# Kernel tuning notes

Measured on AMD Instinct MI355X. Metric: run time of the kernel, lower is better.

The kernel has to match this reference:

```python
import jax, jax.numpy as jnp
import numpy as np

B, T, N, F_IN = 32, 64, 128, 16
H, SOUT = 64, 16
D = N * SOUT            # transformer d_model = 2048
NHEADS, DH = 16, 128
DFF, LAYERS = 2048, 2
NCLASSES, OUT = 8, 10
THR = 0.004             # edge threshold on sigmoid(V)/N


def setup_inputs():
    key = jax.random.key(0)
    ks = iter(jax.random.split(key, 40))
    r = lambda *s: jax.random.normal(next(ks), s, jnp.float32) * 0.02
    return {
        'X': jax.random.normal(next(ks), (B, T, N * F_IN), jnp.float32),
        'V_Adap': jax.random.normal(next(ks), (NCLASSES, N, N), jnp.float32),
        'Wl': r(F_IN, H), 'bl': jnp.zeros((H,)),
        'Wr': r(F_IN, H), 'br': jnp.zeros((H,)),
        'att': jax.random.normal(next(ks), (H,), jnp.float32) * 0.1,
        'gat_bias': jnp.zeros((H,)),
        'Wfc': r(H, SOUT), 'bfc': jnp.zeros((SOUT,)),
        'Wq': r(LAYERS, D, D), 'bq': jnp.zeros((LAYERS, D)),
        'Wk': r(LAYERS, D, D), 'bk': jnp.zeros((LAYERS, D)),
        'Wv': r(LAYERS, D, D), 'bv': jnp.zeros((LAYERS, D)),
        'Wo': r(LAYERS, D, D), 'bo': jnp.zeros((LAYERS, D)),
        'ln1_g': jnp.ones((LAYERS, D)), 'ln1_b': jnp.zeros((LAYERS, D)),
        'W1': r(LAYERS, D, DFF), 'b1': jnp.zeros((LAYERS, DFF)),
        'W2': r(LAYERS, DFF, D), 'b2': jnp.zeros((LAYERS, D)),
        'ln2_g': jnp.ones((LAYERS, D)), 'ln2_b': jnp.zeros((LAYERS, D)),
        'Wout': r(D, OUT), 'bout': jnp.zeros((OUT,)),
        'class_idx': 2,
    }


def _ln(x, g, b):
    mu = jnp.mean(x, -1, keepdims=True)
    var = jnp.var(x, -1, keepdims=True)
    return (x - mu) / jnp.sqrt(var + 1e-5) * g + b


def reference(X, V_Adap, Wl, bl, Wr, br, att, gat_bias, Wfc, bfc,
              Wq, bq, Wk, bk, Wv, bv, Wo, bo, ln1_g, ln1_b,
              W1, b1, W2, b2, ln2_g, ln2_b, Wout, bout, class_idx):
    # dynamic adjacency: sigmoid + scale + threshold (data-dependent sparsity as a mask)
    A = jax.nn.sigmoid(V_Adap[class_idx]) / N
    mask = (A > THR) | jnp.eye(N, dtype=bool)   # GATv2Conv default add_self_loops

    def gat_step(x_t):                           # x_t: (B, N, F_IN)
        xl = x_t @ Wl + bl                       # source transform (B, N, H)
        xr = x_t @ Wr + br                       # target transform (B, N, H)
        s = jax.nn.leaky_relu(xl[:, :, None, :] + xr[:, None, :, :], 0.2)  # (B, src, dst, H)
        e = jnp.where(mask[None], jnp.einsum('bijh,h->bij', s, att), -1e9)
        alpha = jax.nn.softmax(e, axis=1)        # softmax over sources per target node
        out = jnp.einsum('bij,bih->bjh', alpha, xl) + gat_bias
        return out @ Wfc + bfc                   # (B, N, SOUT)

    Xr = X.reshape(B, T, N, F_IN).transpose(1, 0, 2, 3)   # (T, B, N, F)
    spatial = jax.lax.map(gat_step, Xr)                   # (T, B, N, SOUT)
    h = spatial.transpose(1, 0, 2, 3).reshape(B, T, D)

    # post-norm TransformerEncoder (torch defaults: relu, d_ff=2048, no dropout at eval)
    for l in range(LAYERS):
        q = (h @ Wq[l] + bq[l]).reshape(B, T, NHEADS, DH).transpose(0, 2, 1, 3)
        k = (h @ Wk[l] + bk[l]).reshape(B, T, NHEADS, DH).transpose(0, 2, 1, 3)
        v = (h @ Wv[l] + bv[l]).reshape(B, T, NHEADS, DH).transpose(0, 2, 1, 3)
        aw = jax.nn.softmax(jnp.einsum('bhqd,bhkd->bhqk', q, k) / np.float32(np.sqrt(DH)), axis=-1)
        ao = jnp.einsum('bhqk,bhkd->bhqd', aw, v).transpose(0, 2, 1, 3).reshape(B, T, D)
        h = _ln(h + ao @ Wo[l] + bo[l], ln1_g[l], ln1_b[l])
        ff = jax.nn.relu(h @ W1[l] + b1[l]) @ W2[l] + b2[l]
        h = _ln(h + ff, ln2_g[l], ln2_b[l])

    return h[:, -1, :] @ Wout + bout             # (B, OUT)
```

## Files before the change

### kernel.cpp

```cpp
#include <hip/hip_runtime.h>
#include <cstdint>
#include <cstddef>


typedef unsigned short u16;
typedef __bf16 bf16x8 __attribute__((ext_vector_type(8)));
typedef float f32x4 __attribute__((ext_vector_type(4)));
typedef float f32x2 __attribute__((ext_vector_type(2)));
typedef unsigned int u32x4 __attribute__((ext_vector_type(4)));
typedef float f32x4v __attribute__((ext_vector_type(4)));
typedef unsigned short u16x4 __attribute__((ext_vector_type(4)));

__device__ __forceinline__ u16 f2b(float f) {
  union { float f; unsigned u; } x; x.f = f;
  unsigned r = x.u + 0x7fffu + ((x.u >> 16) & 1u);
  return (u16)(r >> 16);
}
__device__ __forceinline__ float b2f(u16 s) {
  union { unsigned u; float f; } x; x.u = ((unsigned)s) << 16;
  return x.f;
}
__device__ __forceinline__ float b2f_lo(unsigned q) {
  union { unsigned u; float f; } x; x.u = q << 16;
  return x.f;
}
__device__ __forceinline__ float b2f_hi(unsigned q) {
  union { unsigned u; float f; } x; x.u = q & 0xffff0000u;
  return x.f;
}

__device__ __forceinline__ void gload_lds16(const void* g, void* l) {
  __builtin_amdgcn_global_load_lds(
      (const __attribute__((address_space(1))) unsigned int*)g,
      (__attribute__((address_space(3))) unsigned int*)l, 16, 0, 0);
}

__global__ __launch_bounds__(1024) void gat_kernel(
    const float* __restrict__ X, const float* __restrict__ V_Adap,
    const int* __restrict__ class_idx,
    const float* __restrict__ Wl, const float* __restrict__ bl,
    const float* __restrict__ Wr, const float* __restrict__ br,
    const float* __restrict__ att, const float* __restrict__ gat_bias,
    const float* __restrict__ Wfc, const float* __restrict__ bfc,
    float* __restrict__ h_f32, u16* __restrict__ h_b16)
{
  const int bt = blockIdx.x;
  const int tid = threadIdx.x;

  __shared__ __align__(16) float xlT[64 * 132];
  __shared__ __align__(16) float xrT[64 * 132];
  __shared__ __align__(16) u16   xlTb[64 * 136];
  __shared__ __align__(16) u16   esbT[128 * 136];
  __shared__ __align__(16) u16   aggb[128 * 72];
  __shared__ __align__(16) float WlT[64 * 20];
  __shared__ __align__(16) float WrT[64 * 20];
  __shared__ __align__(16) float WfcT[16 * 66];
  __shared__ float atts[64], bls[64], brs[64], gbias[64], bfcs[16];
  __shared__ float cls[128], crs[128], inv_s[128];
  __shared__ float red[8 * 128];

  float* scratchX = (float*)aggb;

  {
    const int h = tid >> 4, f = tid & 15;
    WlT[h * 20 + f] = Wl[f * 64 + h];
    WrT[h * 20 + f] = Wr[f * 64 + h];
    WfcT[f * 66 + h] = Wfc[h * 16 + f];
  }
  if (tid < 64) { atts[tid] = att[tid]; bls[tid] = bl[tid]; brs[tid] = br[tid]; gbias[tid] = gat_bias[tid]; }
  if (tid < 16) bfcs[tid] = bfc[tid];
  if (tid < 512)
    ((f32x4*)scratchX)[tid] = ((const f32x4*)(X + (size_t)bt * 2048))[tid];
  const int cidx = *class_idx;
  __syncthreads();

  {
    const int h = tid & 63, ng = tid >> 6;
    f32x4 wl4[4], wr4[4];
    #pragma unroll
    for (int f4 = 0; f4 < 4; f4++) {
      wl4[f4] = *(const f32x4*)&WlT[h * 20 + f4 * 4];
      wr4[f4] = *(const f32x4*)&WrT[h * 20 + f4 * 4];
    }
    const float blh = bls[h], brh = brs[h];
    float al8[8], ar8[8];
    #pragma unroll
    for (int t = 0; t < 8; t++) {
      const int n = ng * 8 + t;
      float al = blh, ar = brh;
      #pragma unroll
      for (int f4 = 0; f4 < 4; f4++) {
        const f32x4 xv = *(const f32x4*)&scratchX[n * 16 + f4 * 4];
        #pragma unroll
        for (int f = 0; f < 4; f++) {
          al = fmaf(xv[f], wl4[f4][f], al);
          ar = fmaf(xv[f], wr4[f4][f], ar);
        }
      }
      al8[t] = al; ar8[t] = ar;
    }
    *(f32x4*)&xlT[h * 132 + ng * 8]     = *(f32x4*)&al8[0];
    *(f32x4*)&xlT[h * 132 + ng * 8 + 4] = *(f32x4*)&al8[4];
    *(f32x4*)&xrT[h * 132 + ng * 8]     = *(f32x4*)&ar8[0];
    *(f32x4*)&xrT[h * 132 + ng * 8 + 4] = *(f32x4*)&ar8[4];
    u16 pb[8];
    #pragma unroll
    for (int t = 0; t < 8; t++) pb[t] = f2b(al8[t]);
    *(u16x4*)&xlTb[h * 136 + ng * 8]     = *(u16x4*)&pb[0];
    *(u16x4*)&xlTb[h * 136 + ng * 8 + 4] = *(u16x4*)&pb[4];
  }
  __syncthreads();

  {
    const int n = tid & 127, g = tid >> 7;
    const float* srcT = (g < 4) ? xlT : xrT;
    const int h0 = (g & 3) * 16;
    float s = 0.f;
    #pragma unroll
    for (int hh = 0; hh < 16; hh++)
      s = fmaf(atts[h0 + hh], srcT[(h0 + hh) * 132 + n], s);
    red[g * 128 + n] = s;
  }
  __syncthreads();
  if (tid < 256) {
    const int n = tid & 127;
    const int base = (tid < 128) ? 0 : 4;
    const float s = ((red[base * 128 + n] + red[(base + 1) * 128 + n])
                   + red[(base + 2) * 128 + n]) + red[(base + 3) * 128 + n];
    if (tid < 128) cls[n] = s; else crs[n] = s;
  }
  __syncthreads();

  {
    const int i0 = (tid >> 6) * 8;
    const int j0 = (tid & 63) * 2;
    float acc[8][2] = {};
    #pragma unroll 8
    for (int h = 0; h < 64; h++) {
      const float ah = att[h];
      const f32x4 xa0 = *(const f32x4*)&xlT[h * 132 + i0];
      const f32x4 xa1 = *(const f32x4*)&xlT[h * 132 + i0 + 4];
      const f32x2 xb  = *(const f32x2*)&xrT[h * 132 + j0];
      #pragma unroll
      for (int a = 0; a < 4; a++) {
        acc[a][0]     = fmaf(ah, __builtin_fabsf(xa0[a] + xb[0]), acc[a][0]);
        acc[a][1]     = fmaf(ah, __builtin_fabsf(xa0[a] + xb[1]), acc[a][1]);
        acc[4 + a][0] = fmaf(ah, __builtin_fabsf(xa1[a] + xb[0]), acc[4 + a][0]);
        acc[4 + a][1] = fmaf(ah, __builtin_fabsf(xa1[a] + xb[1]), acc[4 + a][1]);
      }
    }
    const float* Vc = V_Adap + (size_t)cidx * 16384;
    float vm[8][2];
    #pragma unroll
    for (int a = 0; a < 8; a++) {
      const f32x2 vc = *(const f32x2*)&Vc[(size_t)(i0 + a) * 128 + j0];
      vm[a][0] = vc[0]; vm[a][1] = vc[1];
    }
    const f32x4 cl0 = *(const f32x4*)&cls[i0];
    const f32x4 cl1 = *(const f32x4*)&cls[i0 + 4];
    float cli[8] = {cl0[0], cl0[1], cl0[2], cl0[3], cl1[0], cl1[1], cl1[2], cl1[3]};
    #pragma unroll
    for (int b = 0; b < 2; b++) {
      const int j = j0 + b;
      const float ej = 0.6f * crs[j];
      u16 pk[8];
      #pragma unroll
      for (int a = 0; a < 8; a++) {
        const int i = i0 + a;
        const float e = ej + 0.6f * cli[a] + 0.4f * acc[a][b];
        const bool m = (vm[a][b] > 0.04800922f) || (i == j);
        pk[a] = f2b(m ? e : -1e9f);
      }
      *(u16x4*)&esbT[j * 136 + i0]     = *(u16x4*)&pk[0];
      *(u16x4*)&esbT[j * 136 + i0 + 4] = *(u16x4*)&pk[4];
    }
  }
  __syncthreads();

  {
    const int j = tid >> 3, c = tid & 7;
    u16* rp = &esbT[j * 136 + c * 16];
    float ps = 0.f;
    #pragma unroll
    for (int half = 0; half < 2; half++) {
      u32x4 q = *(u32x4*)(rp + half * 8);
      #pragma unroll
      for (int w2 = 0; w2 < 4; w2++) {
        const float p0 = __expf(b2f_lo(q[w2]));
        const float p1 = __expf(b2f_hi(q[w2]));
        ps += p0 + p1;
        q[w2] = (unsigned)f2b(p0) | ((unsigned)f2b(p1) << 16);
      }
      *(u32x4*)(rp + half * 8) = q;
    }
    red[c * 128 + j] = ps;
  }
  __syncthreads();
  if (tid < 128) {
    float s = 0.f;
    #pragma unroll
    for (int c = 0; c < 8; c++) s += red[c * 128 + tid];
    inv_s[tid] = 1.f / s;
  }
  __syncthreads();

  {
    const int w = tid >> 6, lane = tid & 63;
    const int lq = lane >> 4, lr = lane & 15;
    const int jt = w >> 1, ht0 = (w & 1) * 2;
    f32x4 acc2[2] = {};
    #pragma unroll
    for (int ks = 0; ks < 4; ks++) {
      const bf16x8 af = __builtin_bit_cast(bf16x8,
          *(const u32x4*)&esbT[(jt * 16 + lr) * 136 + ks * 32 + lq * 8]);
      #pragma unroll
      for (int t = 0; t < 2; t++) {
        const bf16x8 bfb = __builtin_bit_cast(bf16x8,
            *(const u32x4*)&xlTb[((ht0 + t) * 16 + lr) * 136 + ks * 32 + lq * 8]);
        acc2[t] = __builtin_amdgcn_mfma_f32_16x16x32_bf16(af, bfb, acc2[t], 0, 0, 0);
      }
    }
    #pragma unroll
    for (int t = 0; t < 2; t++) {
      const int h = (ht0 + t) * 16 + lr;
      const float gb = gbias[h];
      #pragma unroll
      for (int r = 0; r < 4; r++) {
        const int j = jt * 16 + lq * 4 + r;
        aggb[j * 72 + h] = f2b(acc2[t][r] * inv_s[j] + gb);
      }
    }
  }
  __syncthreads();

  {
    const int j = tid >> 3, s0 = (tid & 7) * 2;
    float o0 = bfcs[s0], o1 = bfcs[s0 + 1];
    #pragma unroll
    for (int h8 = 0; h8 < 8; h8++) {
      u32x4 q = *(const u32x4*)&aggb[j * 72 + h8 * 8];
      #pragma unroll
      for (int w2 = 0; w2 < 4; w2++) {
        const int h = h8 * 8 + w2 * 2;
        const float a0 = b2f_lo(q[w2]);
        const float a1 = b2f_hi(q[w2]);
        o0 = fmaf(a0, WfcT[s0 * 66 + h], o0);
        o1 = fmaf(a0, WfcT[(s0 + 1) * 66 + h], o1);
        o0 = fmaf(a1, WfcT[s0 * 66 + h + 1], o0);
        o1 = fmaf(a1, WfcT[(s0 + 1) * 66 + h + 1], o1);
      }
    }
    const size_t off = (size_t)bt * 2048 + j * 16 + s0;
    h_f32[off] = o0; h_f32[off + 1] = o1;
    h_b16[off] = f2b(o0); h_b16[off + 1] = f2b(o1);
  }
}

struct TransArgs {
  const float* s0; const float* s1; const float* s2;
  u16* d0; u16* d1; u16* d2;
};

__global__ __launch_bounds__(256) void transpose_cast(TransArgs p)
{
  const float* src = (blockIdx.z == 0) ? p.s0 : (blockIdx.z == 1) ? p.s1 : p.s2;
  u16* dst = (blockIdx.z == 0) ? p.d0 : (blockIdx.z == 1) ? p.d1 : p.d2;
  __shared__ u16 tile[64][66];
  const int k0 = blockIdx.y * 64, n0 = blockIdx.x * 64;
  const int tid = threadIdx.x;
  const int c = tid & 63, rb = tid >> 6;
  #pragma unroll
  for (int r = 0; r < 16; r++) {
    const int k = rb + r * 4;
    tile[k][c] = f2b(src[(size_t)(k0 + k) * 2048 + n0 + c]);
  }
  __syncthreads();
  #pragma unroll
  for (int r = 0; r < 16; r++) {
    const int n = rb + r * 4;
    dst[(size_t)(n0 + n) * 2048 + k0 + c] = tile[c][n];
  }
}

struct GemmArgs {
  const u16* A;
  const u16* Bt0; const u16* Bt1; const u16* Bt2;
  const float* b0; const float* b1; const float* b2;
  void* C0; void* C1; void* C2;
  int N; int K;
};

template <int MODE>
__global__ __launch_bounds__(256) void gemm_bt(GemmArgs g)
{
  const int z = blockIdx.z;
  const u16* Bt = (z == 0) ? g.Bt0 : (z == 1) ? g.Bt1 : g.Bt2;
  const float* bias = (z == 0) ? g.b0 : (z == 1) ? g.b1 : g.b2;
  void* C = (z == 0) ? g.C0 : (z == 1) ? g.C1 : g.C2;
  const int N = g.N, K = g.K;
  const int m0 = blockIdx.y * 128, n0 = blockIdx.x * 128;

  __shared__ __align__(16) u16 As[3][128 * 32];
  __shared__ __align__(16) u16 Bs[3][128 * 32];

  const int tid = threadIdx.x;
  const int lane = tid & 63, w = tid >> 6;
  const int srow = w * 16 + (lane >> 2);
  const int scol = ((lane & 3) ^ ((lane >> 2) & 3)) * 8;
  const u16* gA = g.A + (size_t)(m0 + srow) * K + scol;
  const u16* gB = Bt + (size_t)(n0 + srow) * K + scol;
  const int lbase = (w * 16) * 32;

  const int wm = (w >> 1) * 64, wn = (w & 1) * 64;
  const int lq = lane >> 4, lr = lane & 15;
  const int csw = (lr & 3) << 3;

  f32x4 acc[4][4] = {};
  const int NT = K >> 5;

  auto stage = [&](int buf, int kt) {
    const int kk = kt << 5;
    #pragma unroll
    for (int c = 0; c < 2; c++) {
      gload_lds16(gA + (size_t)(c * 64) * K + kk, &As[buf][lbase + c * 64 * 32]);
      gload_lds16(gB + (size_t)(c * 64) * K + kk, &Bs[buf][lbase + c * 64 * 32]);
    }
  };
  auto compute = [&](int buf) {
    bf16x8 af[4], bfr[4];
    #pragma unroll
    for (int i = 0; i < 4; i++) {
      af[i] = __builtin_bit_cast(bf16x8,
          *(const u32x4*)&As[buf][(wm + i * 16 + lr) * 32 + ((lq * 8) ^ csw)]);
      bfr[i] = __builtin_bit_cast(bf16x8,
          *(const u32x4*)&Bs[buf][(wn + i * 16 + lr) * 32 + ((lq * 8) ^ csw)]);
    }
    #pragma unroll
    for (int mi = 0; mi < 4; mi++)
      #pragma unroll
      for (int ni = 0; ni < 4; ni++)
        acc[mi][ni] = __builtin_amdgcn_mfma_f32_16x16x32_bf16(af[mi], bfr[ni], acc[mi][ni], 0, 0, 0);
  };

  stage(0, 0);
  stage(1, 1);
  int cA = 0;
  for (int kt = 0; kt < NT; ++kt) {
    if (kt + 2 < NT) {
      int b2 = cA + 2; if (b2 >= 3) b2 -= 3;
      stage(b2, kt + 2);
      asm volatile("s_waitcnt vmcnt(8)" ::: "memory");
    } else if (kt + 1 < NT) {
      asm volatile("s_waitcnt vmcnt(4)" ::: "memory");
    } else {
      asm volatile("s_waitcnt vmcnt(0)" ::: "memory");
    }
    __builtin_amdgcn_s_barrier();
    asm volatile("" ::: "memory");
    __builtin_amdgcn_s_setprio(1);
    compute(cA);
    __builtin_amdgcn_s_setprio(0);
    asm volatile("" ::: "memory");
    __builtin_amdgcn_s_barrier();
    asm volatile("" ::: "memory");
    if (++cA == 3) cA = 0;
  }

  #pragma unroll
  for (int ni = 0; ni < 4; ni++) {
    const int col = n0 + wn + ni * 16 + lr;
    const float bv = bias[col];
    #pragma unroll
    for (int mi = 0; mi < 4; mi++) {
      #pragma unroll
      for (int r = 0; r < 4; r++) {
        const int row = m0 + wm + mi * 16 + lq * 4 + r;
        float v = acc[mi][ni][r] + bv;
        if (MODE == 0) {
          ((float*)C)[(size_t)row * N + col] = v;
        } else {
          if (MODE == 2) v = fmaxf(v, 0.f);
          ((u16*)C)[(size_t)row * N + col] = f2b(v);
        }
      }
    }
  }
}

template <int MODE>
__global__ __launch_bounds__(256) void gemm_bt64(GemmArgs g)
{
  const u16* Bt = g.Bt0;
  const float* bias = g.b0;
  void* C = g.C0;
  const int N = g.N, K = g.K;
  const int m0 = blockIdx.y * 128, n0 = blockIdx.x * 64;

  __shared__ __align__(16) u16 As[3][128 * 64];
  __shared__ __align__(16) u16 Bs[3][64 * 64];

  const int tid = threadIdx.x;
  const int lane = tid & 63, w = tid >> 6;
  const int srow = w * 8 + (lane >> 3);
  const int scol = ((lane & 7) ^ (lane >> 3)) * 8;
  const u16* gA = g.A + (size_t)(m0 + srow) * K + scol;
  const u16* gB = Bt + (size_t)(n0 + srow) * K + scol;
  const int lbase = (w * 8) * 64;

  const int wm = w * 32;
  const int lq = lane >> 4, lr = lane & 15;
  const int csw = (lr & 7) << 3;

  f32x4 acc[2][4] = {};
  const int NT = K >> 6;

  auto stage = [&](int buf, int kt) {
    const int kk = kt << 6;
    #pragma unroll
    for (int c = 0; c < 4; c++)
      gload_lds16(gA + (size_t)(c * 32) * K + kk, &As[buf][lbase + c * 32 * 64]);
    #pragma unroll
    for (int c = 0; c < 2; c++)
      gload_lds16(gB + (size_t)(c * 32) * K + kk, &Bs[buf][lbase + c * 32 * 64]);
  };
  auto compute = [&](int buf) {
    #pragma unroll
    for (int ks = 0; ks < 2; ks++) {
      bf16x8 af[2], bfr[4];
      #pragma unroll
      for (int i = 0; i < 2; i++)
        af[i] = __builtin_bit_cast(bf16x8,
            *(const u32x4*)&As[buf][(wm + i * 16 + lr) * 64 + ((ks * 32 + lq * 8) ^ csw)]);
      #pragma unroll
      for (int i = 0; i < 4; i++)
        bfr[i] = __builtin_bit_cast(bf16x8,
            *(const u32x4*)&Bs[buf][(i * 16 + lr) * 64 + ((ks * 32 + lq * 8) ^ csw)]);
      #pragma unroll
      for (int mi = 0; mi < 2; mi++)
        #pragma unroll
        for (int ni = 0; ni < 4; ni++)
          acc[mi][ni] = __builtin_amdgcn_mfma_f32_16x16x32_bf16(af[mi], bfr[ni], acc[mi][ni], 0, 0, 0);
    }
  };

  stage(0, 0);
  stage(1, 1);
  int cA = 0;
  for (int kt = 0; kt < NT; ++kt) {
    if (kt + 2 < NT) {
      int b2 = cA + 2; if (b2 >= 3) b2 -= 3;
      stage(b2, kt + 2);
      asm volatile("s_waitcnt vmcnt(12)" ::: "memory");
    } else if (kt + 1 < NT) {
      asm volatile("s_waitcnt vmcnt(6)" ::: "memory");
    } else {
      asm volatile("s_waitcnt vmcnt(0)" ::: "memory");
    }
    __builtin_amdgcn_s_barrier();
    asm volatile("" ::: "memory");
    __builtin_amdgcn_s_setprio(1);
    compute(cA);
    __builtin_amdgcn_s_setprio(0);
    asm volatile("" ::: "memory");
    __builtin_amdgcn_s_barrier();
    asm volatile("" ::: "memory");
    if (++cA == 3) cA = 0;
  }

  #pragma unroll
  for (int ni = 0; ni < 4; ni++) {
    const int col = n0 + ni * 16 + lr;
    const float bv = bias[col];
    #pragma unroll
    for (int mi = 0; mi < 2; mi++) {
      #pragma unroll
      for (int r = 0; r < 4; r++) {
        const int row = m0 + wm + mi * 16 + lq * 4 + r;
        float v = acc[mi][ni][r] + bv;
        if (MODE == 0) {
          ((float*)C)[(size_t)row * N + col] = v;
        } else {
          if (MODE == 2) v = fmaxf(v, 0.f);
          ((u16*)C)[(size_t)row * N + col] = f2b(v);
        }
      }
    }
  }
}

__global__ __launch_bounds__(256) void attn_kernel(
    const u16* __restrict__ Qb, const u16* __restrict__ Kb,
    const u16* __restrict__ Vb, u16* __restrict__ AOb)
{
  const int head = blockIdx.x, b = blockIdx.y;
  const int tid = threadIdx.x;
  __shared__ __align__(16) float qs[64 * 132];
  __shared__ __align__(16) float ks[64 * 132];
  __shared__ __align__(16) float vs[64 * 128];
  __shared__ __align__(16) float ss[64 * 65];
  const size_t base = ((size_t)b * 64) * 2048 + (size_t)head * 128;

  for (int idx = tid; idx < 1024; idx += 256) {
    const int t_ = idx >> 4, d8 = (idx & 15) * 8;
    const size_t gp = base + (size_t)t_ * 2048 + d8;
    const u32x4 q = *(const u32x4*)(Qb + gp);
    const u32x4 k = *(const u32x4*)(Kb + gp);
    const u32x4 v = *(const u32x4*)(Vb + gp);
    f32x4 q0 = {b2f_lo(q[0]), b2f_hi(q[0]), b2f_lo(q[1]), b2f_hi(q[1])};
    f32x4 q1 = {b2f_lo(q[2]), b2f_hi(q[2]), b2f_lo(q[3]), b2f_hi(q[3])};
    f32x4 k0 = {b2f_lo(k[0]), b2f_hi(k[0]), b2f_lo(k[1]), b2f_hi(k[1])};
    f32x4 k1 = {b2f_lo(k[2]), b2f_hi(k[2]), b2f_lo(k[3]), b2f_hi(k[3])};
    f32x4 v0 = {b2f_lo(v[0]), b2f_hi(v[0]), b2f_lo(v[1]), b2f_hi(v[1])};
    f32x4 v1 = {b2f_lo(v[2]), b2f_hi(v[2]), b2f_lo(v[3]), b2f_hi(v[3])};
    *(f32x4*)&qs[t_ * 132 + d8] = q0; *(f32x4*)&qs[t_ * 132 + d8 + 4] = q1;
    *(f32x4*)&ks[t_ * 132 + d8] = k0; *(f32x4*)&ks[t_ * 132 + d8 + 4] = k1;
    *(f32x4*)&vs[t_ * 128 + d8] = v0; *(f32x4*)&vs[t_ * 128 + d8 + 4] = v1;
  }
  __syncthreads();

  {
    const int i0 = (tid >> 4) * 4, j0 = tid & 15;
    float acc[4][4] = {};
    #pragma unroll 2
    for (int d0 = 0; d0 < 128; d0 += 4) {
      f32x4 qv[4], kv[4];
      #pragma unroll
      for (int a = 0; a < 4; a++) qv[a] = *(const f32x4*)&qs[(i0 + a) * 132 + d0];
      #pragma unroll
      for (int c = 0; c < 4; c++) kv[c] = *(const f32x4*)&ks[(j0 + c * 16) * 132 + d0];
      #pragma unroll
      for (int a = 0; a < 4; a++)
        #pragma unroll
        for (int c = 0; c < 4; c++)
          #pragma unroll
          for (int e = 0; e < 4; e++)
            acc[a][c] = fmaf(qv[a][e], kv[c][e], acc[a][c]);
    }
    const float sc = 0.08838834764831845f;
    #pragma unroll
    for (int a = 0; a < 4; a++)
      #pragma unroll
      for (int c = 0; c < 4; c++)
        ss[(i0 + a) * 65 + j0 + c * 16] = acc[a][c] * sc;
  }
  __syncthreads();

  {
    const int row = tid >> 2;
    float* rp = &ss[row * 65 + (tid & 3) * 16];
    float mx = -3e38f;
    #pragma unroll
    for (int j = 0; j < 16; j++) mx = fmaxf(mx, rp[j]);
    mx = fmaxf(mx, __shfl_xor(mx, 1, 64));
    mx = fmaxf(mx, __shfl_xor(mx, 2, 64));
    float s = 0.f;
    #pragma unroll
    for (int j = 0; j < 16; j++) { const float p = __expf(rp[j] - mx); rp[j] = p; s += p; }
    s += __shfl_xor(s, 1, 64);
    s += __shfl_xor(s, 2, 64);
    const float inv = 1.f / s;
    #pragma unroll
    for (int j = 0; j < 16; j++) rp[j] *= inv;
  }
  __syncthreads();

  {
    const int i0 = (tid >> 4) * 4, d0 = (tid & 15) * 8;
    float o[4][8] = {};
    for (int j = 0; j < 64; j++) {
      float pv[4];
      #pragma unroll
      for (int a = 0; a < 4; a++) pv[a] = ss[(i0 + a) * 65 + j];
      f32x4v v0 = *(const f32x4v*)&vs[j * 128 + d0];
      f32x4v v1 = *(const f32x4v*)&vs[j * 128 + d0 + 4];
      float vv[8] = {v0[0], v0[1], v0[2], v0[3], v1[0], v1[1], v1[2], v1[3]};
      #pragma unroll
      for (int a = 0; a < 4; a++)
        #pragma unroll
        for (int c = 0; c < 8; c++)
          o[a][c] = fmaf(pv[a], vv[c], o[a][c]);
    }
    #pragma unroll
    for (int a = 0; a < 4; a++)
      #pragma unroll
      for (int c = 0; c < 8; c++)
        AOb[base + (size_t)(i0 + a) * 2048 + d0 + c] = f2b(o[a][c]);
  }
}

__global__ __launch_bounds__(256) void ln_kernel(
    const float* __restrict__ hin, const float* __restrict__ delta,
    const float* __restrict__ gamma, const float* __restrict__ beta,
    float* __restrict__ hout, u16* __restrict__ bout_)
{
  const int token = blockIdx.x, tid = threadIdx.x;
  const size_t off = (size_t)token * 2048;
  __shared__ float red[8];
  f32x4 v[2];
  float s = 0.f;
  #pragma unroll
  for (int r = 0; r < 2; r++) {
    const int i = r * 1024 + tid * 4;
    const f32x4 a = *(const f32x4*)(hin + off + i);
    const f32x4 b = *(const f32x4*)(delta + off + i);
    v[r] = a + b;
    s += v[r][0] + v[r][1] + v[r][2] + v[r][3];
  }
  #pragma unroll
  for (int o = 32; o > 0; o >>= 1) s += __shfl_down(s, o, 64);
  if ((tid & 63) == 0) red[tid >> 6] = s;
  __syncthreads();
  const float mean = (red[0] + red[1] + red[2] + red[3]) * (1.f / 2048.f);
  float s2 = 0.f;
  #pragma unroll
  for (int r = 0; r < 2; r++)
    #pragma unroll
    for (int e = 0; e < 4; e++) { const float d = v[r][e] - mean; s2 = fmaf(d, d, s2); }
  #pragma unroll
  for (int o = 32; o > 0; o >>= 1) s2 += __shfl_down(s2, o, 64);
  if ((tid & 63) == 0) red[4 + (tid >> 6)] = s2;
  __syncthreads();
  const float var = (red[4] + red[5] + red[6] + red[7]) * (1.f / 2048.f);
  const float rstd = rsqrtf(var + 1e-5f);
  #pragma unroll
  for (int r = 0; r < 2; r++) {
    const int i = r * 1024 + tid * 4;
    const f32x4 gm = *(const f32x4*)(gamma + i);
    const f32x4 bt = *(const f32x4*)(beta + i);
    f32x4 y;
    u16x4 pb;
    #pragma unroll
    for (int e = 0; e < 4; e++) {
      y[e] = (v[r][e] - mean) * rstd * gm[e] + bt[e];
      pb[e] = f2b(y[e]);
    }
    *(f32x4*)(hout + off + i) = y;
    *(u16x4*)(bout_ + off + i) = pb;
  }
}

__global__ __launch_bounds__(256) void final_kernel(
    const float* __restrict__ h, const float* __restrict__ Wout,
    const float* __restrict__ bout, float* __restrict__ out)
{
  const int b = blockIdx.x, tid = threadIdx.x;
  __shared__ float row[2048];
  __shared__ float part[256];
  const float* hr = h + ((size_t)b * 64 + 63) * 2048;
  for (int i = tid; i < 2048; i += 256) row[i] = hr[i];
  __syncthreads();
  const int o = tid & 15, ch = tid >> 4;
  float s = 0.f;
  if (o < 10) {
    const int i0 = ch * 128;
    for (int i = i0; i < i0 + 128; i++) s = fmaf(row[i], Wout[(size_t)i * 10 + o], s);
  }
  part[tid] = s;
  __syncthreads();
  if (tid < 10) {
    float t = bout[tid];
    for (int c2 = 0; c2 < 16; c2++) t += part[c2 * 16 + tid];
    out[(size_t)b * 10 + tid] = t;
  }
}

extern "C" void kernel_launch(void* const* d_in, const int* in_sizes, int n_in,
                              void* d_out, int out_size, void* d_ws, size_t ws_size,
                              hipStream_t stream)
{
  const float* X        = (const float*)d_in[0];
  const float* V_Adap   = (const float*)d_in[1];
  const float* Wl       = (const float*)d_in[2];
  const float* bl       = (const float*)d_in[3];
  const float* Wr       = (const float*)d_in[4];
  const float* br       = (const float*)d_in[5];
  const float* att      = (const float*)d_in[6];
  const float* gat_bias = (const float*)d_in[7];
  const float* Wfc      = (const float*)d_in[8];
  const float* bfc      = (const float*)d_in[9];
  const float* Wq       = (const float*)d_in[10];
  const float* bq       = (const float*)d_in[11];
  const float* Wk       = (const float*)d_in[12];
  const float* bk       = (const float*)d_in[13];
  const float* Wv       = (const float*)d_in[14];
  const float* bv       = (const float*)d_in[15];
  const float* Wo       = (const float*)d_in[16];
  const float* bo       = (const float*)d_in[17];
  const float* ln1_g    = (const float*)d_in[18];
  const float* ln1_b    = (const float*)d_in[19];
  const float* W1       = (const float*)d_in[20];
  const float* b1       = (const float*)d_in[21];
  const float* W2       = (const float*)d_in[22];
  const float* b2       = (const float*)d_in[23];
  const float* ln2_g    = (const float*)d_in[24];
  const float* ln2_b    = (const float*)d_in[25];
  const float* WoutP    = (const float*)d_in[26];
  const float* boutP    = (const float*)d_in[27];
  const int*   class_idx = (const int*)d_in[28];

  char* ws = (char*)d_ws;
  const size_t MB = (size_t)1 << 20;
  float* h_f32 = (float*)(ws);
  u16*   h_b16 = (u16*)(ws + 16 * MB);
  u16*   Qb    = (u16*)(ws + 24 * MB);
  u16*   Kb    = (u16*)(ws + 32 * MB);
  u16*   Vb    = (u16*)(ws + 40 * MB);
  u16*   AOb   = (u16*)(ws + 48 * MB);
  float* tmp   = (float*)(ws + 56 * MB);
  u16*   ff1b  = (u16*)(ws + 72 * MB);
  u16*   Wt0   = (u16*)(ws + 80 * MB);
  u16*   Wt1   = (u16*)(ws + 88 * MB);
  u16*   Wt2   = (u16*)(ws + 96 * MB);

  gat_kernel<<<2048, 1024, 0, stream>>>(X, V_Adap, class_idx, Wl, bl, Wr, br,
                                        att, gat_bias, Wfc, bfc, h_f32, h_b16);

  const size_t DD = 2048ull * 2048ull;
  for (int l = 0; l < 2; l++) {
    const size_t wofs = (size_t)l * DD;
    const size_t bofs = (size_t)l * 2048;

    transpose_cast<<<dim3(32, 32, 3), 256, 0, stream>>>(
        TransArgs{Wq + wofs, Wk + wofs, Wv + wofs, Wt0, Wt1, Wt2});
    gemm_bt<1><<<dim3(16, 16, 3), 256, 0, stream>>>(
        GemmArgs{h_b16, Wt0, Wt1, Wt2, bq + bofs, bk + bofs, bv + bofs,
                 Qb, Kb, Vb, 2048, 2048});

    attn_kernel<<<dim3(16, 32), 256, 0, stream>>>(Qb, Kb, Vb, AOb);

    transpose_cast<<<dim3(32, 32, 3), 256, 0, stream>>>(
        TransArgs{Wo + wofs, W1 + wofs, W2 + wofs, Wt0, Wt1, Wt2});

    gemm_bt64<0><<<dim3(32, 16), 256, 0, stream>>>(
        GemmArgs{AOb, Wt0, nullptr, nullptr, bo + bofs, nullptr, nullptr,
                 tmp, nullptr, nullptr, 2048, 2048});
    ln_kernel<<<2048, 256, 0, stream>>>(h_f32, tmp, ln1_g + bofs, ln1_b + bofs,
                                        h_f32, h_b16);

    gemm_bt64<2><<<dim3(32, 16), 256, 0, stream>>>(
        GemmArgs{h_b16, Wt1, nullptr, nullptr, b1 + bofs, nullptr, nullptr,
                 ff1b, nullptr, nullptr, 2048, 2048});

    gemm_bt64<0><<<dim3(32, 16), 256, 0, stream>>>(
        GemmArgs{ff1b, Wt2, nullptr, nullptr, b2 + bofs, nullptr, nullptr,
                 tmp, nullptr, nullptr, 2048, 2048});
    ln_kernel<<<2048, 256, 0, stream>>>(h_f32, tmp, ln2_g + bofs, ln2_b + bofs,
                                        h_f32, h_b16);
  }

  final_kernel<<<32, 256, 0, stream>>>(h_f32, WoutP, boutP, (float*)d_out);
}
```

Before: 874.4 us.

## Split-K output GEMMs, swizzle GEMM grids, MFMA attention scores, fuse GAT softmax exp

Several independent changes land together. The Wo and W2 projections now use a new split-K GEMM (gemm_bt64sk) that writes two fp32 partial sums, and the LayerNorm kernel adds both partials into the residual. This doubles the number of blocks for those GEMMs. Both existing GEMMs get a blockIdx swizzle that groups tiles for better L2 reuse. Attention QK^T now keeps Q and K in bf16 shared memory and computes scores with MFMA instead of scalar fp32 FMAs. In the GAT kernel the exp and masking move into the edge-score pass, which drops one shared-memory pass and one barrier. The exp now runs on the unshifted scores with no max subtraction, and the attention scores lose some precision from bf16.

```diff
diff --git a/kernel.cpp b/kernel.cpp
--- a/kernel.cpp
+++ b/kernel.cpp
@@ -60,6 +60,7 @@
   __shared__ float red[8 * 128];
 
   float* scratchX = (float*)aggb;
+  float* red2 = (float*)aggb;
 
   {
     const int h = tid >> 4, f = tid & 15;
@@ -132,7 +133,8 @@
   __syncthreads();
 
   {
-    const int i0 = (tid >> 6) * 8;
+    const int w = tid >> 6;
+    const int i0 = w * 8;
     const int j0 = (tid & 63) * 2;
     float acc[8][2] = {};
     #pragma unroll 8
@@ -159,47 +161,33 @@
     const f32x4 cl0 = *(const f32x4*)&cls[i0];
     const f32x4 cl1 = *(const f32x4*)&cls[i0 + 4];
     float cli[8] = {cl0[0], cl0[1], cl0[2], cl0[3], cl1[0], cl1[1], cl1[2], cl1[3]};
+    float psum[2];
     #pragma unroll
     for (int b = 0; b < 2; b++) {
       const int j = j0 + b;
       const float ej = 0.6f * crs[j];
       u16 pk[8];
+      float ps = 0.f;
       #pragma unroll
       for (int a = 0; a < 8; a++) {
         const int i = i0 + a;
         const float e = ej + 0.6f * cli[a] + 0.4f * acc[a][b];
         const bool m = (vm[a][b] > 0.04800922f) || (i == j);
-        pk[a] = f2b(m ? e : -1e9f);
-      }
+        const float p = m ? __expf(e) : 0.f;
+        ps += p;
+        pk[a] = f2b(p);
+      }
+      psum[b] = ps;
       *(u16x4*)&esbT[j * 136 + i0]     = *(u16x4*)&pk[0];
       *(u16x4*)&esbT[j * 136 + i0 + 4] = *(u16x4*)&pk[4];
     }
-  }
-  __syncthreads();
-
-  {
-    const int j = tid >> 3, c = tid & 7;
-    u16* rp = &esbT[j * 136 + c * 16];
-    float ps = 0.f;
-    #pragma unroll
-    for (int half = 0; half < 2; half++) {
-      u32x4 q = *(u32x4*)(rp + half * 8);
-      #pragma unroll
-      for (int w2 = 0; w2 < 4; w2++) {
-        const float p0 = __expf(b2f_lo(q[w2]));
-        const float p1 = __expf(b2f_hi(q[w2]));
-        ps += p0 + p1;
-        q[w2] = (unsigned)f2b(p0) | ((unsigned)f2b(p1) << 16);
-      }
-      *(u32x4*)(rp + half * 8) = q;
-    }
-    red[c * 128 + j] = ps;
+    *(f32x2*)&red2[w * 128 + j0] = *(f32x2*)&psum[0];
   }
   __syncthreads();
   if (tid < 128) {
     float s = 0.f;
     #pragma unroll
-    for (int c = 0; c < 8; c++) s += red[c * 128 + tid];
+    for (int c = 0; c < 16; c++) s += red2[c * 128 + tid];
     inv_s[tid] = 1.f / s;
   }
   __syncthreads();
@@ -298,7 +286,11 @@
   const float* bias = (z == 0) ? g.b0 : (z == 1) ? g.b1 : g.b2;
   void* C = (z == 0) ? g.C0 : (z == 1) ? g.C1 : g.C2;
   const int N = g.N, K = g.K;
-  const int m0 = blockIdx.y * 128, n0 = blockIdx.x * 128;
+  const int lin = blockIdx.y * 16 + blockIdx.x;
+  const int xc = lin & 7, xt = lin >> 3;
+  const int wx = (xc & 3) * 4 + (xt & 3);
+  const int wy = (xc >> 2) * 8 + (xt >> 2);
+  const int m0 = wy * 128, n0 = wx * 128;
 
   __shared__ __align__(16) u16 As[3][128 * 32];
   __shared__ __align__(16) u16 Bs[3][128 * 32];
@@ -394,7 +386,11 @@
   const float* bias = g.b0;
   void* C = g.C0;
   const int N = g.N, K = g.K;
-  const int m0 = blockIdx.y * 128, n0 = blockIdx.x * 64;
+  const int lin = blockIdx.y * 32 + blockIdx.x;
+  const int xc = lin & 7, xt = lin >> 3;
+  const int wx = (xc & 3) * 8 + (xt & 7);
+  const int wy = (xc >> 2) * 8 + (xt >> 3);
+  const int m0 = wy * 128, n0 = wx * 64;
 
   __shared__ __align__(16) u16 As[3][128 * 64];
   __shared__ __align__(16) u16 Bs[3][64 * 64];
@@ -488,14 +484,109 @@
   }
 }
 
+__global__ __launch_bounds__(256) void gemm_bt64sk(
+    const u16* __restrict__ A, const u16* __restrict__ Bt,
+    const float* __restrict__ bias, float* __restrict__ C0,
+    float* __restrict__ C1, int N, int K)
+{
+  const int z = blockIdx.z;
+  float* C = z ? C1 : C0;
+  const int khalf = K >> 1;
+  const int lin = blockIdx.y * 32 + blockIdx.x;
+  const int xc = lin & 7, xt = lin >> 3;
+  const int wx = (xc & 3) * 8 + (xt & 7);
+  const int wy = (xc >> 2) * 8 + (xt >> 3);
+  const int m0 = wy * 128, n0 = wx * 64;
+
+  __shared__ __align__(16) u16 As[3][128 * 32];
+  __shared__ __align__(16) u16 Bs[3][64 * 32];
+
+  const int tid = threadIdx.x;
+  const int lane = tid & 63, w = tid >> 6;
+  const int srow = w * 16 + (lane >> 2);
+  const int scol = ((lane & 3) ^ ((lane >> 2) & 3)) * 8;
+  const u16* gA = A + (size_t)(m0 + srow) * K + (size_t)z * khalf + scol;
+  const u16* gB = Bt + (size_t)(n0 + srow) * K + (size_t)z * khalf + scol;
+  const int lbaseA = (w * 16) * 32;
+  const int lbaseB = (w * 16) * 32;
+
+  const int wm = w * 32;
+  const int lq = lane >> 4, lr = lane & 15;
+  const int csw = (lr & 3) << 3;
+
+  f32x4 acc[2][4] = {};
+  const int NT = khalf >> 5;
+
+  auto stage = [&](int buf, int kt) {
+    const int kk = kt << 5;
+    gload_lds16(gA + kk, &As[buf][lbaseA]);
+    gload_lds16(gA + (size_t)64 * K + kk, &As[buf][lbaseA + 64 * 32]);
+    gload_lds16(gB + kk, &Bs[buf][lbaseB]);
+  };
+  auto compute = [&](int buf) {
+    bf16x8 af[2], bfr[4];
+    #pragma unroll
+    for (int i = 0; i < 2; i++)
+      af[i] = __builtin_bit_cast(bf16x8,
+          *(const u32x4*)&As[buf][(wm + i * 16 + lr) * 32 + ((lq * 8) ^ csw)]);
+    #pragma unroll
+    for (int i = 0; i < 4; i++)
+      bfr[i] = __builtin_bit_cast(bf16x8,
+          *(const u32x4*)&Bs[buf][(i * 16 + lr) * 32 + ((lq * 8) ^ csw)]);
+    #pragma unroll
+    for (int mi = 0; mi < 2; mi++)
+      #pragma unroll
+      for (int ni = 0; ni < 4; ni++)
+        acc[mi][ni] = __builtin_amdgcn_mfma_f32_16x16x32_bf16(af[mi], bfr[ni], acc[mi][ni], 0, 0, 0);
+  };
+
+  stage(0, 0);
+  stage(1, 1);
+  int cA = 0;
+  for (int kt = 0; kt < NT; ++kt) {
+    if (kt + 2 < NT) {
+      int b2 = cA + 2; if (b2 >= 3) b2 -= 3;
+      stage(b2, kt + 2);
+      asm volatile("s_waitcnt vmcnt(6)" ::: "memory");
+    } else if (kt + 1 < NT) {
+      asm volatile("s_waitcnt vmcnt(3)" ::: "memory");
+    } else {
+      asm volatile("s_waitcnt vmcnt(0)" ::: "memory");
+    }
+    __builtin_amdgcn_s_barrier();
+    asm volatile("" ::: "memory");
+    __builtin_amdgcn_s_setprio(1);
+    compute(cA);
+    __builtin_amdgcn_s_setprio(0);
+    asm volatile("" ::: "memory");
+    __builtin_amdgcn_s_barrier();
+    asm volatile("" ::: "memory");
+    if (++cA == 3) cA = 0;
+  }
+
+  #pragma unroll
+  for (int ni = 0; ni < 4; ni++) {
+    const int col = n0 + ni * 16 + lr;
+    const float bv = z ? 0.f : bias[col];
+    #pragma unroll
+    for (int mi = 0; mi < 2; mi++) {
+      #pragma unroll
+      for (int r = 0; r < 4; r++) {
+        const int row = m0 + wm + mi * 16 + lq * 4 + r;
+        C[(size_t)row * N + col] = acc[mi][ni][r] + bv;
+      }
+    }
+  }
+}
+
 __global__ __launch_bounds__(256) void attn_kernel(
     const u16* __restrict__ Qb, const u16* __restrict__ Kb,
     const u16* __restrict__ Vb, u16* __restrict__ AOb)
 {
   const int head = blockIdx.x, b = blockIdx.y;
   const int tid = threadIdx.x;
-  __shared__ __align__(16) float qs[64 * 132];
-  __shared__ __align__(16) float ks[64 * 132];
+  __shared__ __align__(16) u16   qs16[64 * 136];
+  __shared__ __align__(16) u16   ks16[64 * 136];
   __shared__ __align__(16) float vs[64 * 128];
   __shared__ __align__(16) float ss[64 * 65];
   const size_t base = ((size_t)b * 64) * 2048 + (size_t)head * 128;
@@ -506,42 +597,35 @@
     const u32x4 q = *(const u32x4*)(Qb + gp);
     const u32x4 k = *(const u32x4*)(Kb + gp);
     const u32x4 v = *(const u32x4*)(Vb + gp);
-    f32x4 q0 = {b2f_lo(q[0]), b2f_hi(q[0]), b2f_lo(q[1]), b2f_hi(q[1])};
-    f32x4 q1 = {b2f_lo(q[2]), b2f_hi(q[2]), b2f_lo(q[3]), b2f_hi(q[3])};
-    f32x4 k0 = {b2f_lo(k[0]), b2f_hi(k[0]), b2f_lo(k[1]), b2f_hi(k[1])};
-    f32x4 k1 = {b2f_lo(k[2]), b2f_hi(k[2]), b2f_lo(k[3]), b2f_hi(k[3])};
+    *(u32x4*)&qs16[t_ * 136 + d8] = q;
+    *(u32x4*)&ks16[t_ * 136 + d8] = k;
     f32x4 v0 = {b2f_lo(v[0]), b2f_hi(v[0]), b2f_lo(v[1]), b2f_hi(v[1])};
     f32x4 v1 = {b2f_lo(v[2]), b2f_hi(v[2]), b2f_lo(v[3]), b2f_hi(v[3])};
-    *(f32x4*)&qs[t_ * 132 + d8] = q0; *(f32x4*)&qs[t_ * 132 + d8 + 4] = q1;
-    *(f32x4*)&ks[t_ * 132 + d8] = k0; *(f32x4*)&ks[t_ * 132 + d8 + 4] = k1;
     *(f32x4*)&vs[t_ * 128 + d8] = v0; *(f32x4*)&vs[t_ * 128 + d8 + 4] = v1;
   }
   __syncthreads();
 
   {
-    const int i0 = (tid >> 4) * 4, j0 = tid & 15;
-    float acc[4][4] = {};
-    #pragma unroll 2
-    for (int d0 = 0; d0 < 128; d0 += 4) {
-      f32x4 qv[4], kv[4];
-      #pragma unroll
-      for (int a = 0; a < 4; a++) qv[a] = *(const f32x4*)&qs[(i0 + a) * 132 + d0];
-      #pragma unroll
-      for (int c = 0; c < 4; c++) kv[c] = *(const f32x4*)&ks[(j0 + c * 16) * 132 + d0];
-      #pragma unroll
-      for (int a = 0; a < 4; a++)
-        #pragma unroll
-        for (int c = 0; c < 4; c++)
-          #pragma unroll
-          for (int e = 0; e < 4; e++)
-            acc[a][c] = fmaf(qv[a][e], kv[c][e], acc[a][c]);
+    const int w = tid >> 6, lane = tid & 63;
+    const int lq = lane >> 4, lr = lane & 15;
+    f32x4 acc4[4] = {};
+    #pragma unroll
+    for (int ks = 0; ks < 4; ks++) {
+      const bf16x8 kf = __builtin_bit_cast(bf16x8,
+          *(const u32x4*)&ks16[(w * 16 + lr) * 136 + ks * 32 + lq * 8]);
+      #pragma unroll
+      for (int mi = 0; mi < 4; mi++) {
+        const bf16x8 qf = __builtin_bit_cast(bf16x8,
+            *(const u32x4*)&qs16[(mi * 16 + lr) * 136 + ks * 32 + lq * 8]);
+        acc4[mi] = __builtin_amdgcn_mfma_f32_16x16x32_bf16(qf, kf, acc4[mi], 0, 0, 0);
+      }
     }
     const float sc = 0.08838834764831845f;
     #pragma unroll
-    for (int a = 0; a < 4; a++)
-      #pragma unroll
-      for (int c = 0; c < 4; c++)
-        ss[(i0 + a) * 65 + j0 + c * 16] = acc[a][c] * sc;
+    for (int mi = 0; mi < 4; mi++)
+      #pragma unroll
+      for (int r = 0; r < 4; r++)
+        ss[(mi * 16 + lq * 4 + r) * 65 + w * 16 + lr] = acc4[mi][r] * sc;
   }
   __syncthreads();
 
@@ -589,7 +673,8 @@
 }
 
 __global__ __launch_bounds__(256) void ln_kernel(
-    const float* __restrict__ hin, const float* __restrict__ delta,
+    const float* __restrict__ hin, const float* __restrict__ d0,
+    const float* __restrict__ d1,
     const float* __restrict__ gamma, const float* __restrict__ beta,
     float* __restrict__ hout, u16* __restrict__ bout_)
 {
@@ -602,8 +687,9 @@
   for (int r = 0; r < 2; r++) {
     const int i = r * 1024 + tid * 4;
     const f32x4 a = *(const f32x4*)(hin + off + i);
-    const f32x4 b = *(const f32x4*)(delta + off + i);
-    v[r] = a + b;
+    const f32x4 b0 = *(const f32x4*)(d0 + off + i);
+    const f32x4 b1 = *(const f32x4*)(d1 + off + i);
+    v[r] = a + b0 + b1;
     s += v[r][0] + v[r][1] + v[r][2] + v[r][3];
   }
   #pragma unroll
@@ -711,6 +797,8 @@
   u16*   Wt0   = (u16*)(ws + 80 * MB);
   u16*   Wt1   = (u16*)(ws + 88 * MB);
   u16*   Wt2   = (u16*)(ws + 96 * MB);
+  float* P0 = (float*)(ws + 24 * MB);
+  float* P1 = tmp;
 
   gat_kernel<<<2048, 1024, 0, stream>>>(X, V_Adap, class_idx, Wl, bl, Wr, br,
                                         att, gat_bias, Wfc, bfc, h_f32, h_b16);
@@ -731,20 +819,18 @@
     transpose_cast<<<dim3(32, 32, 3), 256, 0, stream>>>(
         TransArgs{Wo + wofs, W1 + wofs, W2 + wofs, Wt0, Wt1, Wt2});
 
-    gemm_bt64<0><<<dim3(32, 16), 256, 0, stream>>>(
-        GemmArgs{AOb, Wt0, nullptr, nullptr, bo + bofs, nullptr, nullptr,
-                 tmp, nullptr, nullptr, 2048, 2048});
-    ln_kernel<<<2048, 256, 0, stream>>>(h_f32, tmp, ln1_g + bofs, ln1_b + bofs,
+    gemm_bt64sk<<<dim3(32, 16, 2), 256, 0, stream>>>(
+        AOb, Wt0, bo + bofs, P0, P1, 2048, 2048);
+    ln_kernel<<<2048, 256, 0, stream>>>(h_f32, P0, P1, ln1_g + bofs, ln1_b + bofs,
                                         h_f32, h_b16);
 
     gemm_bt64<2><<<dim3(32, 16), 256, 0, stream>>>(
         GemmArgs{h_b16, Wt1, nullptr, nullptr, b1 + bofs, nullptr, nullptr,
                  ff1b, nullptr, nullptr, 2048, 2048});
 
-    gemm_bt64<0><<<dim3(32, 16), 256, 0, stream>>>(
-        GemmArgs{ff1b, Wt2, nullptr, nullptr, b2 + bofs, nullptr, nullptr,
-                 tmp, nullptr, nullptr, 2048, 2048});
-    ln_kernel<<<2048, 256, 0, stream>>>(h_f32, tmp, ln2_g + bofs, ln2_b + bofs,
+    gemm_bt64sk<<<dim3(32, 16, 2), 256, 0, stream>>>(
+        ff1b, Wt2, b2 + bofs, P0, P1, 2048, 2048);
+    ln_kernel<<<2048, 256, 0, stream>>>(h_f32, P0, P1, ln2_g + bofs, ln2_b + bofs,
                                         h_f32, h_b16);
   }
 
```

Measured after the change: 873.0 us. About the same (-0.2%).

## Fuse QKV into one 256x256-tile GEMM, MFMA attention scores, fused GAT exp

Applied to the files above, without the earlier changes.

Replaces the three-way batched QKV GEMM with a single GEMM over a concatenated [6144 x 2048] weight using 256x256 tiles and 512 threads, writing an interleaved QKV buffer. It also adds a tile-swizzled block ordering for L2 locality. The attention kernel now keeps Q and K in bf16 in LDS and computes QK^T with MFMA instead of scalar FP32. The GAT kernel computes exp directly while building the masked scores, which removes one pass and one barrier. These changes target GEMM efficiency, attention compute and extra LDS passes, at the cost of higher register and LDS pressure in the larger tile.

```diff
diff --git a/kernel.cpp b/kernel.cpp
--- a/kernel.cpp
+++ b/kernel.cpp
@@ -60,6 +60,7 @@
   __shared__ float red[8 * 128];
 
   float* scratchX = (float*)aggb;
+  float* red2 = (float*)aggb;
 
   {
     const int h = tid >> 4, f = tid & 15;
@@ -132,7 +133,8 @@
   __syncthreads();
 
   {
-    const int i0 = (tid >> 6) * 8;
+    const int w = tid >> 6;
+    const int i0 = w * 8;
     const int j0 = (tid & 63) * 2;
     float acc[8][2] = {};
     #pragma unroll 8
@@ -159,47 +161,33 @@
     const f32x4 cl0 = *(const f32x4*)&cls[i0];
     const f32x4 cl1 = *(const f32x4*)&cls[i0 + 4];
     float cli[8] = {cl0[0], cl0[1], cl0[2], cl0[3], cl1[0], cl1[1], cl1[2], cl1[3]};
+    float psum[2];
     #pragma unroll
     for (int b = 0; b < 2; b++) {
       const int j = j0 + b;
       const float ej = 0.6f * crs[j];
       u16 pk[8];
+      float ps = 0.f;
       #pragma unroll
       for (int a = 0; a < 8; a++) {
         const int i = i0 + a;
         const float e = ej + 0.6f * cli[a] + 0.4f * acc[a][b];
         const bool m = (vm[a][b] > 0.04800922f) || (i == j);
-        pk[a] = f2b(m ? e : -1e9f);
-      }
+        const float p = m ? __expf(e) : 0.f;
+        ps += p;
+        pk[a] = f2b(p);
+      }
+      psum[b] = ps;
       *(u16x4*)&esbT[j * 136 + i0]     = *(u16x4*)&pk[0];
       *(u16x4*)&esbT[j * 136 + i0 + 4] = *(u16x4*)&pk[4];
     }
-  }
-  __syncthreads();
-
-  {
-    const int j = tid >> 3, c = tid & 7;
-    u16* rp = &esbT[j * 136 + c * 16];
-    float ps = 0.f;
-    #pragma unroll
-    for (int half = 0; half < 2; half++) {
-      u32x4 q = *(u32x4*)(rp + half * 8);
-      #pragma unroll
-      for (int w2 = 0; w2 < 4; w2++) {
-        const float p0 = __expf(b2f_lo(q[w2]));
-        const float p1 = __expf(b2f_hi(q[w2]));
-        ps += p0 + p1;
-        q[w2] = (unsigned)f2b(p0) | ((unsigned)f2b(p1) << 16);
-      }
-      *(u32x4*)(rp + half * 8) = q;
-    }
-    red[c * 128 + j] = ps;
+    *(f32x2*)&red2[w * 128 + j0] = *(f32x2*)&psum[0];
   }
   __syncthreads();
   if (tid < 128) {
     float s = 0.f;
     #pragma unroll
-    for (int c = 0; c < 8; c++) s += red[c * 128 + tid];
+    for (int c = 0; c < 16; c++) s += red2[c * 128 + tid];
     inv_s[tid] = 1.f / s;
   }
   __syncthreads();
@@ -282,64 +270,58 @@
   }
 }
 
-struct GemmArgs {
-  const u16* A;
-  const u16* Bt0; const u16* Bt1; const u16* Bt2;
-  const float* b0; const float* b1; const float* b2;
-  void* C0; void* C1; void* C2;
-  int N; int K;
-};
-
-template <int MODE>
-__global__ __launch_bounds__(256) void gemm_bt(GemmArgs g)
+__global__ __launch_bounds__(512) void qkv_gemm(
+    const u16* __restrict__ A, const u16* __restrict__ Bt,
+    const float* __restrict__ bq, const float* __restrict__ bk,
+    const float* __restrict__ bv, u16* __restrict__ C)
 {
-  const int z = blockIdx.z;
-  const u16* Bt = (z == 0) ? g.Bt0 : (z == 1) ? g.Bt1 : g.Bt2;
-  const float* bias = (z == 0) ? g.b0 : (z == 1) ? g.b1 : g.b2;
-  void* C = (z == 0) ? g.C0 : (z == 1) ? g.C1 : g.C2;
-  const int N = g.N, K = g.K;
-  const int m0 = blockIdx.y * 128, n0 = blockIdx.x * 128;
-
-  __shared__ __align__(16) u16 As[3][128 * 32];
-  __shared__ __align__(16) u16 Bs[3][128 * 32];
+  const int K = 2048;
+  const int lin = blockIdx.y * 24 + blockIdx.x;
+  const int xc = lin & 7, xt = lin >> 3;
+  const int wx = xc * 3 + (xt >> 3);
+  const int wy = xt & 7;
+  const int m0 = wy * 256, n0 = wx * 256;
+
+  __shared__ __align__(16) u16 As[3][256 * 32];
+  __shared__ __align__(16) u16 Bs[3][256 * 32];
 
   const int tid = threadIdx.x;
   const int lane = tid & 63, w = tid >> 6;
-  const int srow = w * 16 + (lane >> 2);
+  const int srow = w * 32 + (lane >> 2);
   const int scol = ((lane & 3) ^ ((lane >> 2) & 3)) * 8;
-  const u16* gA = g.A + (size_t)(m0 + srow) * K + scol;
+  const u16* gA = A + (size_t)(m0 + srow) * K + scol;
   const u16* gB = Bt + (size_t)(n0 + srow) * K + scol;
-  const int lbase = (w * 16) * 32;
-
-  const int wm = (w >> 1) * 64, wn = (w & 1) * 64;
+  const int lbase = (w * 32) * 32;
+
+  const int wm = (w >> 2) * 128, wn = (w & 3) * 64;
   const int lq = lane >> 4, lr = lane & 15;
   const int csw = (lr & 3) << 3;
 
-  f32x4 acc[4][4] = {};
+  f32x4 acc[8][4] = {};
   const int NT = K >> 5;
 
   auto stage = [&](int buf, int kt) {
     const int kk = kt << 5;
     #pragma unroll
     for (int c = 0; c < 2; c++) {
-      gload_lds16(gA + (size_t)(c * 64) * K + kk, &As[buf][lbase + c * 64 * 32]);
-      gload_lds16(gB + (size_t)(c * 64) * K + kk, &Bs[buf][lbase + c * 64 * 32]);
+      gload_lds16(gA + (size_t)(c * 16) * K + kk, &As[buf][lbase + c * 16 * 32]);
+      gload_lds16(gB + (size_t)(c * 16) * K + kk, &Bs[buf][lbase + c * 16 * 32]);
     }
   };
   auto compute = [&](int buf) {
-    bf16x8 af[4], bfr[4];
-    #pragma unroll
-    for (int i = 0; i < 4; i++) {
-      af[i] = __builtin_bit_cast(bf16x8,
-          *(const u32x4*)&As[buf][(wm + i * 16 + lr) * 32 + ((lq * 8) ^ csw)]);
+    bf16x8 bfr[4];
+    #pragma unroll
+    for (int i = 0; i < 4; i++)
       bfr[i] = __builtin_bit_cast(bf16x8,
           *(const u32x4*)&Bs[buf][(wn + i * 16 + lr) * 32 + ((lq * 8) ^ csw)]);
-    }
-    #pragma unroll
-    for (int mi = 0; mi < 4; mi++)
+    #pragma unroll
+    for (int mi = 0; mi < 8; mi++) {
+      const bf16x8 af = __builtin_bit_cast(bf16x8,
+          *(const u32x4*)&As[buf][(wm + mi * 16 + lr) * 32 + ((lq * 8) ^ csw)]);
       #pragma unroll
       for (int ni = 0; ni < 4; ni++)
-        acc[mi][ni] = __builtin_amdgcn_mfma_f32_16x16x32_bf16(af[mi], bfr[ni], acc[mi][ni], 0, 0, 0);
+        acc[mi][ni] = __builtin_amdgcn_mfma_f32_16x16x32_bf16(af, bfr[ni], acc[mi][ni], 0, 0, 0);
+    }
   };
 
   stage(0, 0);
@@ -366,26 +348,31 @@
     if (++cA == 3) cA = 0;
   }
 
+  const int seg = n0 >> 11;
+  const float* bias = (seg == 0) ? bq : (seg == 1) ? bk : bv;
+  const int nloc0 = (n0 & 2047) + wn;
   #pragma unroll
   for (int ni = 0; ni < 4; ni++) {
+    const float bvv = bias[nloc0 + ni * 16 + lr];
     const int col = n0 + wn + ni * 16 + lr;
-    const float bv = bias[col];
-    #pragma unroll
-    for (int mi = 0; mi < 4; mi++) {
+    #pragma unroll
+    for (int mi = 0; mi < 8; mi++) {
       #pragma unroll
       for (int r = 0; r < 4; r++) {
         const int row = m0 + wm + mi * 16 + lq * 4 + r;
-        float v = acc[mi][ni][r] + bv;
-        if (MODE == 0) {
-          ((float*)C)[(size_t)row * N + col] = v;
-        } else {
-          if (MODE == 2) v = fmaxf(v, 0.f);
-          ((u16*)C)[(size_t)row * N + col] = f2b(v);
-        }
-      }
-    }
-  }
-}
+        C[(size_t)row * 6144 + col] = f2b(acc[mi][ni][r] + bvv);
+      }
+    }
+  }
+}
+
+struct GemmArgs {
+  const u16* A;
+  const u16* Bt0; const u16* Bt1; const u16* Bt2;
+  const float* b0; const float* b1; const float* b2;
+  void* C0; void* C1; void* C2;
+  int N; int K;
+};
 
 template <int MODE>
 __global__ __launch_bounds__(256) void gemm_bt64(GemmArgs g)
@@ -394,7 +381,11 @@
   const float* bias = g.b0;
   void* C = g.C0;
   const int N = g.N, K = g.K;
-  const int m0 = blockIdx.y * 128, n0 = blockIdx.x * 64;
+  const int lin = blockIdx.y * 32 + blockIdx.x;
+  const int xc = lin & 7, xt = lin >> 3;
+  const int wx = (xc & 3) * 8 + (xt & 7);
+  const int wy = (xc >> 2) * 8 + (xt >> 3);
+  const int m0 = wy * 128, n0 = wx * 64;
 
   __shared__ __align__(16) u16 As[3][128 * 64];
   __shared__ __align__(16) u16 Bs[3][64 * 64];
@@ -489,59 +480,52 @@
 }
 
 __global__ __launch_bounds__(256) void attn_kernel(
-    const u16* __restrict__ Qb, const u16* __restrict__ Kb,
-    const u16* __restrict__ Vb, u16* __restrict__ AOb)
+    const u16* __restrict__ QKV, u16* __restrict__ AOb)
 {
   const int head = blockIdx.x, b = blockIdx.y;
   const int tid = threadIdx.x;
-  __shared__ __align__(16) float qs[64 * 132];
-  __shared__ __align__(16) float ks[64 * 132];
+  __shared__ __align__(16) u16   qs16[64 * 136];
+  __shared__ __align__(16) u16   ks16[64 * 136];
   __shared__ __align__(16) float vs[64 * 128];
   __shared__ __align__(16) float ss[64 * 65];
-  const size_t base = ((size_t)b * 64) * 2048 + (size_t)head * 128;
+  const size_t qbase = ((size_t)b * 64) * 6144 + (size_t)head * 128;
+  const size_t obase = ((size_t)b * 64) * 2048 + (size_t)head * 128;
 
   for (int idx = tid; idx < 1024; idx += 256) {
     const int t_ = idx >> 4, d8 = (idx & 15) * 8;
-    const size_t gp = base + (size_t)t_ * 2048 + d8;
-    const u32x4 q = *(const u32x4*)(Qb + gp);
-    const u32x4 k = *(const u32x4*)(Kb + gp);
-    const u32x4 v = *(const u32x4*)(Vb + gp);
-    f32x4 q0 = {b2f_lo(q[0]), b2f_hi(q[0]), b2f_lo(q[1]), b2f_hi(q[1])};
-    f32x4 q1 = {b2f_lo(q[2]), b2f_hi(q[2]), b2f_lo(q[3]), b2f_hi(q[3])};
-    f32x4 k0 = {b2f_lo(k[0]), b2f_hi(k[0]), b2f_lo(k[1]), b2f_hi(k[1])};
-    f32x4 k1 = {b2f_lo(k[2]), b2f_hi(k[2]), b2f_lo(k[3]), b2f_hi(k[3])};
+    const size_t gp = qbase + (size_t)t_ * 6144 + d8;
+    const u32x4 q = *(const u32x4*)(QKV + gp);
+    const u32x4 k = *(const u32x4*)(QKV + gp + 2048);
+    const u32x4 v = *(const u32x4*)(QKV + gp + 4096);
+    *(u32x4*)&qs16[t_ * 136 + d8] = q;
+    *(u32x4*)&ks16[t_ * 136 + d8] = k;
     f32x4 v0 = {b2f_lo(v[0]), b2f_hi(v[0]), b2f_lo(v[1]), b2f_hi(v[1])};
     f32x4 v1 = {b2f_lo(v[2]), b2f_hi(v[2]), b2f_lo(v[3]), b2f_hi(v[3])};
-    *(f32x4*)&qs[t_ * 132 + d8] = q0; *(f32x4*)&qs[t_ * 132 + d8 + 4] = q1;
-    *(f32x4*)&ks[t_ * 132 + d8] = k0; *(f32x4*)&ks[t_ * 132 + d8 + 4] = k1;
     *(f32x4*)&vs[t_ * 128 + d8] = v0; *(f32x4*)&vs[t_ * 128 + d8 + 4] = v1;
   }
   __syncthreads();
 
   {
-    const int i0 = (tid >> 4) * 4, j0 = tid & 15;
-    float acc[4][4] = {};
-    #pragma unroll 2
-    for (int d0 = 0; d0 < 128; d0 += 4) {
-      f32x4 qv[4], kv[4];
-      #pragma unroll
-      for (int a = 0; a < 4; a++) qv[a] = *(const f32x4*)&qs[(i0 + a) * 132 + d0];
-      #pragma unroll
-      for (int c = 0; c < 4; c++) kv[c] = *(const f32x4*)&ks[(j0 + c * 16) * 132 + d0];
-      #pragma unroll
-      for (int a = 0; a < 4; a++)
-        #pragma unroll
-        for (int c = 0; c < 4; c++)
-          #pragma unroll
-          for (int e = 0; e < 4; e++)
-            acc[a][c] = fmaf(qv[a][e], kv[c][e], acc[a][c]);
+    const int w = tid >> 6, lane = tid & 63;
+    const int lq = lane >> 4, lr = lane & 15;
+    f32x4 acc4[4] = {};
+    #pragma unroll
+    for (int ks = 0; ks < 4; ks++) {
+      const bf16x8 kf = __builtin_bit_cast(bf16x8,
+          *(const u32x4*)&ks16[(w * 16 + lr) * 136 + ks * 32 + lq * 8]);
+      #pragma unroll
+      for (int mi = 0; mi < 4; mi++) {
+        const bf16x8 qf = __builtin_bit_cast(bf16x8,
+            *(const u32x4*)&qs16[(mi * 16 + lr) * 136 + ks * 32 + lq * 8]);
+        acc4[mi] = __builtin_amdgcn_mfma_f32_16x16x32_bf16(qf, kf, acc4[mi], 0, 0, 0);
+      }
     }
     const float sc = 0.08838834764831845f;
     #pragma unroll
-    for (int a = 0; a < 4; a++)
-      #pragma unroll
-      for (int c = 0; c < 4; c++)
-        ss[(i0 + a) * 65 + j0 + c * 16] = acc[a][c] * sc;
+    for (int mi = 0; mi < 4; mi++)
+      #pragma unroll
+      for (int r = 0; r < 4; r++)
+        ss[(mi * 16 + lq * 4 + r) * 65 + w * 16 + lr] = acc4[mi][r] * sc;
   }
   __syncthreads();
 
@@ -584,7 +568,7 @@
     for (int a = 0; a < 4; a++)
       #pragma unroll
       for (int c = 0; c < 8; c++)
-        AOb[base + (size_t)(i0 + a) * 2048 + d0 + c] = f2b(o[a][c]);
+        AOb[obase + (size_t)(i0 + a) * 2048 + d0 + c] = f2b(o[a][c]);
   }
 }
 
@@ -702,9 +686,7 @@
   const size_t MB = (size_t)1 << 20;
   float* h_f32 = (float*)(ws);
   u16*   h_b16 = (u16*)(ws + 16 * MB);
-  u16*   Qb    = (u16*)(ws + 24 * MB);
-  u16*   Kb    = (u16*)(ws + 32 * MB);
-  u16*   Vb    = (u16*)(ws + 40 * MB);
+  u16*   QKVb  = (u16*)(ws + 24 * MB);
   u16*   AOb   = (u16*)(ws + 48 * MB);
   float* tmp   = (float*)(ws + 56 * MB);
   u16*   ff1b  = (u16*)(ws + 72 * MB);
@@ -722,11 +704,10 @@
 
     transpose_cast<<<dim3(32, 32, 3), 256, 0, stream>>>(
         TransArgs{Wq + wofs, Wk + wofs, Wv + wofs, Wt0, Wt1, Wt2});
-    gemm_bt<1><<<dim3(16, 16, 3), 256, 0, stream>>>(
-        GemmArgs{h_b16, Wt0, Wt1, Wt2, bq + bofs, bk + bofs, bv + bofs,
-                 Qb, Kb, Vb, 2048, 2048});
-
-    attn_kernel<<<dim3(16, 32), 256, 0, stream>>>(Qb, Kb, Vb, AOb);
+    qkv_gemm<<<dim3(24, 8), 512, 0, stream>>>(
+        h_b16, Wt0, bq + bofs, bk + bofs, bv + bofs, QKVb);
+
+    attn_kernel<<<dim3(16, 32), 256, 0, stream>>>(QKVb, AOb);
 
     transpose_cast<<<dim3(32, 32, 3), 256, 0, stream>>>(
         TransArgs{Wo + wofs, W1 + wofs, W2 + wofs, Wt0, Wt1, Wt2});
```

Measured after the change: 904.8 us. 1.03x slower.
